# Kernel tuning notes

Hardware: AMD Instinct MI355X
Metric: run time of the kernel (lower is better)

The kernel has to match this reference:

```python
import jax, jax.numpy as jnp
import numpy as np

B, T, D, HD = 8, 2048, 1024, 64

def setup_inputs() -> dict:
    key = jax.random.key(0)
    k1, k2, k3, k4 = jax.random.split(key, 4)
    x = jax.random.normal(k1, (B, T, D), dtype=jnp.float32)
    Wq = jax.random.normal(k2, (D, HD), dtype=jnp.float32) * (D ** -0.5)
    Wk = jax.random.normal(k3, (D, HD), dtype=jnp.float32) * (D ** -0.5)
    Wv = jax.random.normal(k4, (D, HD), dtype=jnp.float32) * (D ** -0.5)
    return {"x": x, "Wq": Wq, "Wk": Wk, "Wv": Wv}

def reference(x, Wq, Wk, Wv):
    # x: [B,T,D]; projections: [D,HD]
    q = jnp.einsum('btd,dh->bth', x, Wq)
    k = jnp.einsum('btd,dh->bth', x, Wk)
    v = jnp.einsum('btd,dh->bth', x, Wv)
    hd = q.shape[-1]
    scores = jnp.einsum('bth,bsh->bts', q, k) * (hd ** -0.5)  # [B,T,T]
    t = scores.shape[-1]
    causal = jnp.tril(jnp.ones((t, t), dtype=bool))
    scores = jnp.where(causal, scores, -jnp.inf)
    w = jax.nn.softmax(scores, axis=-1)
    # dropout p=0.0 (eval) -> identity
    return jnp.einsum('bts,bsh->bth', w, v)
```

## Files before the change

### kernel.cpp

```cpp
#include <hip/hip_runtime.h>
#include <hip/hip_bf16.h>
#include <stdint.h>

#define NB 8
#define TT 2048
#define DD 1024
#define HDIM 64

typedef __bf16 bf16x8 __attribute__((ext_vector_type(8)));
typedef float f32x4 __attribute__((ext_vector_type(4)));

static_assert(sizeof(bf16x8) == 16, "bf16x8 must be 16 bytes");

__device__ inline ushort f2bf_bits(float f) {
    __hip_bfloat16 h = __float2bfloat16(f);
    return *reinterpret_cast<ushort*>(&h);
}
__device__ inline float bfbits2f(ushort u) {
    unsigned v = ((unsigned)u) << 16;
    return __builtin_bit_cast(float, v);
}
__device__ inline bf16x8 ldb8(const ushort* p) {
    return *reinterpret_cast<const bf16x8*>(p);
}

typedef __attribute__((address_space(3))) uint32_t lds_u32;
typedef const __attribute__((address_space(1))) uint32_t glb_u32;
__device__ inline void gl_lds16(const void* g, void* l) {
    __builtin_amdgcn_global_load_lds((glb_u32*)g, (lds_u32*)l, 16, 0, 0);
}

#define WCNT_VM2   0xF72
#define WCNT_VM3   0xF73
#define WCNT_VM4   0xF74
#define WCNT_LGKM0 0xC07F

__device__ inline int probe_f32(const ushort* x) {
    int lane = threadIdx.x & 63;
    int wild = 0;
    #pragma unroll
    for (int j = 0; j < 4; ++j) {
        ushort u = x[(lane * 4 + j) * 32];
        int e = (u >> 7) & 0xFF;
        wild += (e >= 0xC0);
    }
    unsigned long long m = __ballot(wild > 0);
    return __popcll(m) > 8;
}

__global__ __launch_bounds__(256) void k_wt(const ushort* __restrict__ x,
                                            const void* __restrict__ Wq,
                                            const void* __restrict__ Wk,
                                            const void* __restrict__ Wv,
                                            ushort* __restrict__ Wt) {
    int f32m = probe_f32(x);
    int idx = blockIdx.x * 256 + threadIdx.x;
    int mat = idx >> 16;
    int rem = idx & 65535;
    int d = rem >> 6;
    int h = rem & 63;
    const void* W = (mat == 0) ? Wq : (mat == 1) ? Wk : Wv;
    float v;
    if (f32m) v = ((const float*)W)[rem];
    else      v = bfbits2f(((const ushort*)W)[rem]);
    if (mat == 0) v *= 0.18033688011112042f;
    Wt[(size_t)mat * 65536 + (size_t)h * DD + d] = f2bf_bits(v);
}

template <int F32M>
__device__ inline void proj_body(const void* __restrict__ xv,
                                 const ushort* __restrict__ Wt,
                                 ushort* __restrict__ Qw,
                                 ushort* __restrict__ Kw,
                                 ushort* __restrict__ Vtw,
                                 ushort* Bf, float* Af) {
    int tid  = threadIdx.x;
    int w    = tid >> 6;
    int lane = tid & 63;
    int quad = lane >> 4;
    int col  = lane & 15;
    int mt   = w >> 2;
    int nh   = w & 3;
    int m0   = blockIdx.x * 32;

    ushort* Afb = (ushort*)Af;

    auto stage = [&](int buf, int kkk) {
        #pragma unroll
        for (int j = 0; j < 3; ++j) {
            int f  = w * 3 + j;
            int nt = f >> 1, ks = f & 1;
            gl_lds16(Wt + (size_t)(nt * 16 + col) * DD + kkk + ks * 32 + quad * 8,
                     Bf + ((size_t)buf * 24 + f) * 512);
        }
        if (F32M) {
            int amt = w >> 2, ks = (w >> 1) & 1, hf = w & 1;
            gl_lds16((const float*)xv + (size_t)(m0 + amt * 16 + col) * DD
                         + kkk + ks * 32 + hf * 4 + quad * 8,
                     Af + ((((buf * 2 + amt) * 2 + ks) * 2) + hf) * 256);
        } else if (w < 4) {
            int amt = w >> 1, ks = w & 1;
            gl_lds16((const ushort*)xv + (size_t)(m0 + amt * 16 + col) * DD
                         + kkk + ks * 32 + quad * 8,
                     Afb + (((buf * 2 + amt) * 2) + ks) * 512);
        }
    };

    f32x4 acc[3];
    #pragma unroll
    for (int i = 0; i < 3; ++i) acc[i] = (f32x4){0.f,0.f,0.f,0.f};

    stage(0, 0);
    for (int kk = 0; kk < DD; kk += 64) {
        int p  = (kk >> 6) & 1;
        int kn = (kk + 64 < DD) ? kk + 64 : kk;
        stage(p ^ 1, kn);
        if (F32M) {
            __builtin_amdgcn_s_waitcnt(WCNT_VM4);
        } else {
            if (w < 4) __builtin_amdgcn_s_waitcnt(WCNT_VM4);
            else       __builtin_amdgcn_s_waitcnt(WCNT_VM3);
        }
        __builtin_amdgcn_s_barrier();

        #pragma unroll
        for (int ks = 0; ks < 2; ++ks) {
            bf16x8 a;
            if (F32M) {
                f32x4 alo = *reinterpret_cast<const f32x4*>(Af + ((((p * 2 + mt) * 2 + ks) * 2) + 0) * 256 + lane * 4);
                f32x4 ahi = *reinterpret_cast<const f32x4*>(Af + ((((p * 2 + mt) * 2 + ks) * 2) + 1) * 256 + lane * 4);
                #pragma unroll
                for (int j = 0; j < 4; ++j) { a[j] = (__bf16)alo[j]; a[4+j] = (__bf16)ahi[j]; }
            } else {
                a = ldb8(Afb + (((p * 2 + mt) * 2) + ks) * 512 + lane * 8);
            }
            #pragma unroll
            for (int j = 0; j < 3; ++j) {
                int nt = nh * 3 + j;
                bf16x8 b = ldb8(Bf + ((size_t)p * 24 + nt * 2 + ks) * 512 + lane * 8);
                acc[j] = __builtin_amdgcn_mfma_f32_16x16x32_bf16(a, b, acc[j], 0, 0, 0);
            }
        }
        __builtin_amdgcn_s_waitcnt(WCNT_LGKM0);
        __builtin_amdgcn_s_barrier();
    }

    #pragma unroll
    for (int j = 0; j < 3; ++j) {
        int nt  = nh * 3 + j;
        int mat = nt >> 2;
        int h   = (nt & 3) * 16 + col;
        if (mat == 2) {
            #pragma unroll
            for (int r = 0; r < 4; ++r) {
                int row = m0 + mt * 16 + quad * 4 + r;
                int bb = row >> 11;
                int t  = row & (TT - 1);
                Vtw[(size_t)bb * HDIM * TT + (size_t)h * TT + t] = f2bf_bits(acc[j][r]);
            }
        } else {
            ushort* outp = (mat == 0) ? Qw : Kw;
            #pragma unroll
            for (int r = 0; r < 4; ++r) {
                int row = m0 + mt * 16 + quad * 4 + r;
                outp[(size_t)row * HDIM + h] = f2bf_bits(acc[j][r]);
            }
        }
    }
}

__global__ __launch_bounds__(512) void k_proj(const void* __restrict__ xv,
                                              const ushort* __restrict__ Wt,
                                              ushort* __restrict__ Qw,
                                              ushort* __restrict__ Kw,
                                              ushort* __restrict__ Vtw) {
    __shared__ ushort Bf[2 * 24 * 512];
    __shared__ float  Af[2 * 2 * 2 * 2 * 256];
    if (probe_f32((const ushort*)xv)) proj_body<1>(xv, Wt, Qw, Kw, Vtw, Bf, Af);
    else                              proj_body<0>(xv, Wt, Qw, Kw, Vtw, Bf, Af);
}

__global__ __launch_bounds__(256) void k_attn(const ushort* __restrict__ Qw,
                                              const ushort* __restrict__ Kw,
                                              const ushort* __restrict__ Vtw,
                                              ushort* __restrict__ Po,
                                              float* __restrict__ Pl) {
    int w    = threadIdx.x >> 6;
    int lane = threadIdx.x & 63;
    int quad = lane >> 4;
    int col  = lane & 15;
    int bid  = blockIdx.x;
    int b    = bid & 7;
    int idx  = 79 - (bid >> 3);
    int c, g;
    if (idx < 32)      { c = 0; g = idx; }
    else if (idx < 56) { c = 1; g = idx - 24; }
    else if (idx < 72) { c = 2; g = idx - 40; }
    else               { c = 3; g = idx - 48; }
    int qb = 4 * g + w;
    int m0 = qb * 16;
    int Bq = (qb < 32) ? qb : (qb < 64) ? 2*qb - 32 : (qb < 96) ? 3*qb - 96 : 4*qb - 192;
    int pid = b * 320 + Bq + c;

    const ushort* Qb = Qw + (size_t)b * TT * HDIM;
    const ushort* Kb = Kw + (size_t)b * TT * HDIM;
    const ushort* Vb = Vtw + (size_t)b * HDIM * TT;

    __shared__ ushort KVb[2][8][512];
    __shared__ __hip_bfloat16 Pls[4][16][40];

    auto stageKV = [&](int buf, int s) {
        #pragma unroll
        for (int j = 0; j < 2; ++j) {
            int f = w * 2 + j;
            const ushort* gp;
            if (f < 4) {
                int half = f & 1;
                int ro   = (f >> 1) * 16;
                gp = Kb + (size_t)(s + ro + col) * HDIM + half * 32 + quad * 8;
            } else {
                int vg = f - 4;
                gp = Vb + (size_t)(vg * 16 + col) * TT + s + quad * 8;
            }
            gl_lds16(gp, &KVb[buf][f][0]);
        }
    };

    bf16x8 qf0 = ldb8(Qb + (size_t)(m0 + col) * HDIM + quad * 8);
    bf16x8 qf1 = ldb8(Qb + (size_t)(m0 + col) * HDIM + 32 + quad * 8);

    f32x4 o0 = {0.f,0.f,0.f,0.f};
    f32x4 o1 = {0.f,0.f,0.f,0.f};
    f32x4 o2 = {0.f,0.f,0.f,0.f};
    f32x4 o3 = {0.f,0.f,0.f,0.f};
    float rsum[4] = {0.f, 0.f, 0.f, 0.f};

    const int start = c * 512;
    const int end   = min(start + 512, 64 * g + 64);

    stageKV(0, start);
    for (int s0 = start; s0 < end; s0 += 32) {
        int p  = ((s0 - start) >> 5) & 1;
        int sn = (s0 + 32 < end) ? s0 + 32 : s0;
        stageKV(p ^ 1, sn);
        __builtin_amdgcn_s_waitcnt(WCNT_VM2);
        __builtin_amdgcn_s_barrier();

        if (s0 < m0 + 16) {
            bf16x8 ck0l = ldb8(&KVb[p][0][lane * 8]);
            bf16x8 ck0h = ldb8(&KVb[p][1][lane * 8]);
            bf16x8 ck1l = ldb8(&KVb[p][2][lane * 8]);
            bf16x8 ck1h = ldb8(&KVb[p][3][lane * 8]);

            f32x4 S0 = {0.f,0.f,0.f,0.f};
            f32x4 S1 = {0.f,0.f,0.f,0.f};
            S0 = __builtin_amdgcn_mfma_f32_16x16x32_bf16(qf0, ck0l, S0, 0, 0, 0);
            S0 = __builtin_amdgcn_mfma_f32_16x16x32_bf16(qf1, ck0h, S0, 0, 0, 0);
            S1 = __builtin_amdgcn_mfma_f32_16x16x32_bf16(qf0, ck1l, S1, 0, 0, 0);
            S1 = __builtin_amdgcn_mfma_f32_16x16x32_bf16(qf1, ck1h, S1, 0, 0, 0);

            #pragma unroll
            for (int r = 0; r < 4; ++r) {
                int trow = m0 + quad * 4 + r;
                float aa = (s0 + col      > trow) ? -1e30f : S0[r];
                float dd = (s0 + 16 + col > trow) ? -1e30f : S1[r];
                float p0 = exp2f(aa);
                float p1 = exp2f(dd);
                rsum[r] += p0 + p1;
                Pls[w][quad * 4 + r][col]      = __float2bfloat16(p0);
                Pls[w][quad * 4 + r][16 + col] = __float2bfloat16(p1);
            }
            bf16x8 pf = *reinterpret_cast<const bf16x8*>(&Pls[w][col][quad * 8]);

            bf16x8 cv0 = ldb8(&KVb[p][4][lane * 8]);
            bf16x8 cv1 = ldb8(&KVb[p][5][lane * 8]);
            bf16x8 cv2 = ldb8(&KVb[p][6][lane * 8]);
            bf16x8 cv3 = ldb8(&KVb[p][7][lane * 8]);
            o0 = __builtin_amdgcn_mfma_f32_16x16x32_bf16(pf, cv0, o0, 0, 0, 0);
            o1 = __builtin_amdgcn_mfma_f32_16x16x32_bf16(pf, cv1, o1, 0, 0, 0);
            o2 = __builtin_amdgcn_mfma_f32_16x16x32_bf16(pf, cv2, o2, 0, 0, 0);
            o3 = __builtin_amdgcn_mfma_f32_16x16x32_bf16(pf, cv3, o3, 0, 0, 0);
        }
        __builtin_amdgcn_s_waitcnt(WCNT_LGKM0);
        __builtin_amdgcn_s_barrier();
    }

    #pragma unroll
    for (int off = 1; off < 16; off <<= 1) {
        #pragma unroll
        for (int r = 0; r < 4; ++r)
            rsum[r] += __shfl_xor(rsum[r], off, 64);
    }

    ushort* pb = Po + (size_t)pid * 1024;
    #pragma unroll
    for (int r = 0; r < 4; ++r) {
        int row = quad * 4 + r;
        pb[row * 64 + 0*16 + col] = f2bf_bits(o0[r]);
        pb[row * 64 + 1*16 + col] = f2bf_bits(o1[r]);
        pb[row * 64 + 2*16 + col] = f2bf_bits(o2[r]);
        pb[row * 64 + 3*16 + col] = f2bf_bits(o3[r]);
        if (col == 0) Pl[pid * 16 + row] = rsum[r];
    }
}

__global__ __launch_bounds__(256) void k_merge(const ushort* __restrict__ x,
                                               const ushort* __restrict__ Po,
                                               const float* __restrict__ Pl,
                                               void* __restrict__ outv) {
    int f32m = probe_f32(x);
    int wid  = blockIdx.x * 4 + (threadIdx.x >> 6);
    int lane = threadIdx.x & 63;
    int row  = lane >> 2;
    int g    = lane & 3;
    int b    = wid >> 7;
    int qb   = wid & 127;
    int nch  = (qb >> 5) + 1;
    int Bq   = (qb < 32) ? qb : (qb < 64) ? 2*qb - 32 : (qb < 96) ? 3*qb - 96 : 4*qb - 192;
    int pid0 = b * 320 + Bq;

    float L = 0.f;
    #pragma unroll
    for (int c = 0; c < 4; ++c)
        if (c < nch) L += Pl[(pid0 + c) * 16 + row];
    float inv = 1.0f / L;

    float o[16];
    #pragma unroll
    for (int j = 0; j < 16; ++j) o[j] = 0.f;
    #pragma unroll
    for (int c = 0; c < 4; ++c) {
        if (c < nch) {
            const ushort* p = Po + (size_t)(pid0 + c) * 1024 + row * 64 + g * 16;
            bf16x8 v0 = ldb8(p);
            bf16x8 v1 = ldb8(p + 8);
            #pragma unroll
            for (int j = 0; j < 8; ++j) {
                o[j]     += (float)v0[j];
                o[8 + j] += (float)v1[j];
            }
        }
    }

    size_t obase = ((size_t)b * TT + qb * 16 + row) * HDIM + g * 16;
    if (f32m) {
        float* ob = (float*)outv + obase;
        #pragma unroll
        for (int j = 0; j < 16; ++j) ob[j] = o[j] * inv;
    } else {
        ushort* ob = (ushort*)outv + obase;
        #pragma unroll
        for (int j = 0; j < 16; ++j) ob[j] = f2bf_bits(o[j] * inv);
    }
}

extern "C" void kernel_launch(void* const* d_in, const int* in_sizes, int n_in,
                              void* d_out, int out_size, void* d_ws, size_t ws_size,
                              hipStream_t stream) {
    const ushort* x = (const ushort*)d_in[0];
    ushort* Wt  = (ushort*)d_ws;
    ushort* Qw  = Wt + 3 * HDIM * DD;
    ushort* Kw  = Qw + (size_t)NB * TT * HDIM;
    ushort* Vtw = Kw + (size_t)NB * TT * HDIM;
    ushort* Po  = Vtw + (size_t)NB * TT * HDIM;
    float*  Pl  = (float*)(Po + (size_t)2560 * 1024);

    k_wt   <<<768, 256, 0, stream>>>(x, d_in[1], d_in[2], d_in[3], Wt);
    k_proj <<<512, 512, 0, stream>>>(d_in[0], Wt, Qw, Kw, Vtw);
    k_attn <<<640, 256, 0, stream>>>(Qw, Kw, Vtw, Po, Pl);
    k_merge<<<256, 256, 0, stream>>>(x, Po, Pl, d_out);
}
```

Before: 155.1 us.

## Load projection A-operand directly into registers and double rows per block

The QKV projection kernel stops staging x through LDS. Each wave now loads its A fragments straight from global memory into registers, prefetching the next k-step, while only the weight tiles stay in LDS. Each block covers 64 rows instead of 32, with every wave computing two 16-row tiles, so each weight tile read from LDS feeds twice as many MFMAs and the grid is halved. This cuts LDS traffic and reuses B better, at the cost of more registers, uncoalesced 16-byte global loads per lane, and fewer blocks to fill the GPU.

```diff
diff --git a/kernel.cpp b/kernel.cpp
--- a/kernel.cpp
+++ b/kernel.cpp
@@ -32,7 +32,6 @@
 
 #define WCNT_VM2   0xF72
 #define WCNT_VM3   0xF73
-#define WCNT_VM4   0xF74
 #define WCNT_LGKM0 0xC07F
 
 __device__ inline int probe_f32(const ushort* x) {
@@ -73,111 +72,134 @@
                                  ushort* __restrict__ Qw,
                                  ushort* __restrict__ Kw,
                                  ushort* __restrict__ Vtw,
-                                 ushort* Bf, float* Af) {
+                                 ushort* Bl) {
     int tid  = threadIdx.x;
     int w    = tid >> 6;
     int lane = tid & 63;
     int quad = lane >> 4;
     int col  = lane & 15;
-    int mt   = w >> 2;
+    int mt2  = w >> 2;
     int nh   = w & 3;
-    int m0   = blockIdx.x * 32;
-
-    ushort* Afb = (ushort*)Af;
-
-    auto stage = [&](int buf, int kkk) {
+    int m0   = blockIdx.x * 64;
+    int rbase = m0 + mt2 * 32;
+
+    const float*  xf = (const float*)xv;
+    const ushort* xb = (const ushort*)xv;
+
+    auto stageB = [&](int buf, int kkk) {
         #pragma unroll
         for (int j = 0; j < 3; ++j) {
             int f  = w * 3 + j;
             int nt = f >> 1, ks = f & 1;
             gl_lds16(Wt + (size_t)(nt * 16 + col) * DD + kkk + ks * 32 + quad * 8,
-                     Bf + ((size_t)buf * 24 + f) * 512);
-        }
-        if (F32M) {
-            int amt = w >> 2, ks = (w >> 1) & 1, hf = w & 1;
-            gl_lds16((const float*)xv + (size_t)(m0 + amt * 16 + col) * DD
-                         + kkk + ks * 32 + hf * 4 + quad * 8,
-                     Af + ((((buf * 2 + amt) * 2 + ks) * 2) + hf) * 256);
-        } else if (w < 4) {
-            int amt = w >> 1, ks = w & 1;
-            gl_lds16((const ushort*)xv + (size_t)(m0 + amt * 16 + col) * DD
-                         + kkk + ks * 32 + quad * 8,
-                     Afb + (((buf * 2 + amt) * 2) + ks) * 512);
+                     Bl + ((size_t)buf * 24 + f) * 512);
         }
     };
 
-    f32x4 acc[3];
-    #pragma unroll
-    for (int i = 0; i < 3; ++i) acc[i] = (f32x4){0.f,0.f,0.f,0.f};
-
-    stage(0, 0);
+    f32x4  aC[8];
+    bf16x8 aCb[4];
+
+    auto loadA = [&](int kkk) {
+        #pragma unroll
+        for (int mloc = 0; mloc < 2; ++mloc) {
+            #pragma unroll
+            for (int ks = 0; ks < 2; ++ks) {
+                size_t ro = (size_t)(rbase + mloc * 16 + col) * DD
+                          + kkk + ks * 32 + quad * 8;
+                if (F32M) {
+                    aC[(mloc * 2 + ks) * 2 + 0] = *reinterpret_cast<const f32x4*>(xf + ro);
+                    aC[(mloc * 2 + ks) * 2 + 1] = *reinterpret_cast<const f32x4*>(xf + ro + 4);
+                } else {
+                    aCb[mloc * 2 + ks] = ldb8(xb + ro);
+                }
+            }
+        }
+    };
+
+    f32x4 acc[2][3];
+    #pragma unroll
+    for (int i = 0; i < 2; ++i)
+        #pragma unroll
+        for (int j = 0; j < 3; ++j) acc[i][j] = (f32x4){0.f, 0.f, 0.f, 0.f};
+
+    stageB(0, 0);
+    loadA(0);
     for (int kk = 0; kk < DD; kk += 64) {
         int p  = (kk >> 6) & 1;
         int kn = (kk + 64 < DD) ? kk + 64 : kk;
-        stage(p ^ 1, kn);
+        stageB(p ^ 1, kn);
+        __builtin_amdgcn_s_waitcnt(WCNT_VM3);
+        __builtin_amdgcn_s_barrier();
+
+        bf16x8 af[4];
         if (F32M) {
-            __builtin_amdgcn_s_waitcnt(WCNT_VM4);
+            #pragma unroll
+            for (int i = 0; i < 4; ++i) {
+                f32x4 lo = aC[2 * i], hi = aC[2 * i + 1];
+                bf16x8 t;
+                #pragma unroll
+                for (int jj = 0; jj < 4; ++jj) {
+                    t[jj]     = (__bf16)lo[jj];
+                    t[4 + jj] = (__bf16)hi[jj];
+                }
+                af[i] = t;
+            }
         } else {
-            if (w < 4) __builtin_amdgcn_s_waitcnt(WCNT_VM4);
-            else       __builtin_amdgcn_s_waitcnt(WCNT_VM3);
-        }
-        __builtin_amdgcn_s_barrier();
+            #pragma unroll
+            for (int i = 0; i < 4; ++i) af[i] = aCb[i];
+        }
+        loadA(kn);
 
         #pragma unroll
         for (int ks = 0; ks < 2; ++ks) {
-            bf16x8 a;
-            if (F32M) {
-                f32x4 alo = *reinterpret_cast<const f32x4*>(Af + ((((p * 2 + mt) * 2 + ks) * 2) + 0) * 256 + lane * 4);
-                f32x4 ahi = *reinterpret_cast<const f32x4*>(Af + ((((p * 2 + mt) * 2 + ks) * 2) + 1) * 256 + lane * 4);
-                #pragma unroll
-                for (int j = 0; j < 4; ++j) { a[j] = (__bf16)alo[j]; a[4+j] = (__bf16)ahi[j]; }
-            } else {
-                a = ldb8(Afb + (((p * 2 + mt) * 2) + ks) * 512 + lane * 8);
-            }
             #pragma unroll
             for (int j = 0; j < 3; ++j) {
                 int nt = nh * 3 + j;
-                bf16x8 b = ldb8(Bf + ((size_t)p * 24 + nt * 2 + ks) * 512 + lane * 8);
-                acc[j] = __builtin_amdgcn_mfma_f32_16x16x32_bf16(a, b, acc[j], 0, 0, 0);
-            }
-        }
+                bf16x8 b = ldb8(Bl + ((size_t)p * 24 + nt * 2 + ks) * 512 + lane * 8);
+                acc[0][j] = __builtin_amdgcn_mfma_f32_16x16x32_bf16(af[0 * 2 + ks], b, acc[0][j], 0, 0, 0);
+                acc[1][j] = __builtin_amdgcn_mfma_f32_16x16x32_bf16(af[1 * 2 + ks], b, acc[1][j], 0, 0, 0);
+            }
+        }
+
         __builtin_amdgcn_s_waitcnt(WCNT_LGKM0);
         __builtin_amdgcn_s_barrier();
     }
 
     #pragma unroll
-    for (int j = 0; j < 3; ++j) {
-        int nt  = nh * 3 + j;
-        int mat = nt >> 2;
-        int h   = (nt & 3) * 16 + col;
-        if (mat == 2) {
-            #pragma unroll
-            for (int r = 0; r < 4; ++r) {
-                int row = m0 + mt * 16 + quad * 4 + r;
-                int bb = row >> 11;
-                int t  = row & (TT - 1);
-                Vtw[(size_t)bb * HDIM * TT + (size_t)h * TT + t] = f2bf_bits(acc[j][r]);
-            }
-        } else {
-            ushort* outp = (mat == 0) ? Qw : Kw;
-            #pragma unroll
-            for (int r = 0; r < 4; ++r) {
-                int row = m0 + mt * 16 + quad * 4 + r;
-                outp[(size_t)row * HDIM + h] = f2bf_bits(acc[j][r]);
-            }
-        }
-    }
-}
-
-__global__ __launch_bounds__(512) void k_proj(const void* __restrict__ xv,
-                                              const ushort* __restrict__ Wt,
-                                              ushort* __restrict__ Qw,
-                                              ushort* __restrict__ Kw,
-                                              ushort* __restrict__ Vtw) {
-    __shared__ ushort Bf[2 * 24 * 512];
-    __shared__ float  Af[2 * 2 * 2 * 2 * 256];
-    if (probe_f32((const ushort*)xv)) proj_body<1>(xv, Wt, Qw, Kw, Vtw, Bf, Af);
-    else                              proj_body<0>(xv, Wt, Qw, Kw, Vtw, Bf, Af);
+    for (int mloc = 0; mloc < 2; ++mloc) {
+        #pragma unroll
+        for (int j = 0; j < 3; ++j) {
+            int nt  = nh * 3 + j;
+            int mat = nt >> 2;
+            int h   = (nt & 3) * 16 + col;
+            if (mat == 2) {
+                #pragma unroll
+                for (int r = 0; r < 4; ++r) {
+                    int row = rbase + mloc * 16 + quad * 4 + r;
+                    int bb = row >> 11;
+                    int t  = row & (TT - 1);
+                    Vtw[(size_t)bb * HDIM * TT + (size_t)h * TT + t] = f2bf_bits(acc[mloc][j][r]);
+                }
+            } else {
+                ushort* outp = (mat == 0) ? Qw : Kw;
+                #pragma unroll
+                for (int r = 0; r < 4; ++r) {
+                    int row = rbase + mloc * 16 + quad * 4 + r;
+                    outp[(size_t)row * HDIM + h] = f2bf_bits(acc[mloc][j][r]);
+                }
+            }
+        }
+    }
+}
+
+__global__ __launch_bounds__(512, 4) void k_proj(const void* __restrict__ xv,
+                                                 const ushort* __restrict__ Wt,
+                                                 ushort* __restrict__ Qw,
+                                                 ushort* __restrict__ Kw,
+                                                 ushort* __restrict__ Vtw) {
+    __shared__ ushort Bl[2 * 24 * 512];
+    if (probe_f32((const ushort*)xv)) proj_body<1>(xv, Wt, Qw, Kw, Vtw, Bl);
+    else                              proj_body<0>(xv, Wt, Qw, Kw, Vtw, Bl);
 }
 
 __global__ __launch_bounds__(256) void k_attn(const ushort* __restrict__ Qw,
@@ -366,7 +388,7 @@
     float*  Pl  = (float*)(Po + (size_t)2560 * 1024);
 
     k_wt   <<<768, 256, 0, stream>>>(x, d_in[1], d_in[2], d_in[3], Wt);
-    k_proj <<<512, 512, 0, stream>>>(d_in[0], Wt, Qw, Kw, Vtw);
+    k_proj <<<256, 512, 0, stream>>>(d_in[0], Wt, Qw, Kw, Vtw);
     k_attn <<<640, 256, 0, stream>>>(Qw, Kw, Vtw, Po, Pl);
     k_merge<<<256, 256, 0, stream>>>(x, Po, Pl, d_out);
 }
```

Result: slower. 172.7 us (+11.4%).

## Widen attention KV tile to 64 keys with triple-buffered LDS staging

Applied to the files above, without the earlier changes.

The attention kernel now processes 64 keys per loop step instead of 32, and stages K/V tiles three buffers deep with a prefetch distance of two. The wait count is raised to match the extra loads in flight, and the launch bounds ask for two blocks per CU. The aim is to halve the barrier and synchronisation count per key and hide more global-load latency behind the MFMA work. In exchange, LDS use grows to roughly 57 KB per block, which may limit occupancy. Causal-diagonal tiles also waste more masked work at the coarser granularity.

```diff
diff --git a/kernel.cpp b/kernel.cpp
--- a/kernel.cpp
+++ b/kernel.cpp
@@ -30,9 +30,9 @@
     __builtin_amdgcn_global_load_lds((glb_u32*)g, (lds_u32*)l, 16, 0, 0);
 }
 
-#define WCNT_VM2   0xF72
 #define WCNT_VM3   0xF73
 #define WCNT_VM4   0xF74
+#define WCNT_VM8   0xF78
 #define WCNT_LGKM0 0xC07F
 
 __device__ inline int probe_f32(const ushort* x) {
@@ -180,11 +180,11 @@
     else                              proj_body<0>(xv, Wt, Qw, Kw, Vtw, Bf, Af);
 }
 
-__global__ __launch_bounds__(256) void k_attn(const ushort* __restrict__ Qw,
-                                              const ushort* __restrict__ Kw,
-                                              const ushort* __restrict__ Vtw,
-                                              ushort* __restrict__ Po,
-                                              float* __restrict__ Pl) {
+__global__ __launch_bounds__(256, 2) void k_attn(const ushort* __restrict__ Qw,
+                                                 const ushort* __restrict__ Kw,
+                                                 const ushort* __restrict__ Vtw,
+                                                 ushort* __restrict__ Po,
+                                                 float* __restrict__ Pl) {
     int w    = threadIdx.x >> 6;
     int lane = threadIdx.x & 63;
     int quad = lane >> 4;
@@ -206,21 +206,23 @@
     const ushort* Kb = Kw + (size_t)b * TT * HDIM;
     const ushort* Vb = Vtw + (size_t)b * HDIM * TT;
 
-    __shared__ ushort KVb[2][8][512];
-    __shared__ __hip_bfloat16 Pls[4][16][40];
+    __shared__ ushort KVb[3][16][512];
+    __shared__ ushort Pls[4][16][72];
 
     auto stageKV = [&](int buf, int s) {
         #pragma unroll
-        for (int j = 0; j < 2; ++j) {
-            int f = w * 2 + j;
+        for (int j = 0; j < 4; ++j) {
+            int f = w * 4 + j;
             const ushort* gp;
-            if (f < 4) {
+            if (f < 8) {
+                int ksub = f >> 1;
                 int half = f & 1;
-                int ro   = (f >> 1) * 16;
-                gp = Kb + (size_t)(s + ro + col) * HDIM + half * 32 + quad * 8;
+                gp = Kb + (size_t)(s + ksub * 16 + col) * HDIM + half * 32 + quad * 8;
             } else {
-                int vg = f - 4;
-                gp = Vb + (size_t)(vg * 16 + col) * TT + s + quad * 8;
+                int vf   = f - 8;
+                int hsub = vf >> 1;
+                int kh   = vf & 1;
+                gp = Vb + (size_t)(hsub * 16 + col) * TT + s + kh * 32 + quad * 8;
             }
             gl_lds16(gp, &KVb[buf][f][0]);
         }
@@ -229,57 +231,58 @@
     bf16x8 qf0 = ldb8(Qb + (size_t)(m0 + col) * HDIM + quad * 8);
     bf16x8 qf1 = ldb8(Qb + (size_t)(m0 + col) * HDIM + 32 + quad * 8);
 
-    f32x4 o0 = {0.f,0.f,0.f,0.f};
-    f32x4 o1 = {0.f,0.f,0.f,0.f};
-    f32x4 o2 = {0.f,0.f,0.f,0.f};
-    f32x4 o3 = {0.f,0.f,0.f,0.f};
+    f32x4 o[4];
+    #pragma unroll
+    for (int i = 0; i < 4; ++i) o[i] = (f32x4){0.f,0.f,0.f,0.f};
     float rsum[4] = {0.f, 0.f, 0.f, 0.f};
 
-    const int start = c * 512;
-    const int end   = min(start + 512, 64 * g + 64);
+    const int start  = c * 512;
+    const int end    = min(start + 512, 64 * g + 64);
+    const int nsteps = (end - start) >> 6;
 
     stageKV(0, start);
-    for (int s0 = start; s0 < end; s0 += 32) {
-        int p  = ((s0 - start) >> 5) & 1;
-        int sn = (s0 + 32 < end) ? s0 + 32 : s0;
-        stageKV(p ^ 1, sn);
-        __builtin_amdgcn_s_waitcnt(WCNT_VM2);
+    stageKV(1, (nsteps > 1) ? start + 64 : start);
+    for (int t = 0; t < nsteps; ++t) {
+        int s0 = start + t * 64;
+        int p  = t % 3;
+        int s2 = (t + 2 < nsteps) ? s0 + 128 : s0;
+        stageKV((p + 2) % 3, s2);
+        __builtin_amdgcn_s_waitcnt(WCNT_VM8);
         __builtin_amdgcn_s_barrier();
 
         if (s0 < m0 + 16) {
-            bf16x8 ck0l = ldb8(&KVb[p][0][lane * 8]);
-            bf16x8 ck0h = ldb8(&KVb[p][1][lane * 8]);
-            bf16x8 ck1l = ldb8(&KVb[p][2][lane * 8]);
-            bf16x8 ck1h = ldb8(&KVb[p][3][lane * 8]);
-
-            f32x4 S0 = {0.f,0.f,0.f,0.f};
-            f32x4 S1 = {0.f,0.f,0.f,0.f};
-            S0 = __builtin_amdgcn_mfma_f32_16x16x32_bf16(qf0, ck0l, S0, 0, 0, 0);
-            S0 = __builtin_amdgcn_mfma_f32_16x16x32_bf16(qf1, ck0h, S0, 0, 0, 0);
-            S1 = __builtin_amdgcn_mfma_f32_16x16x32_bf16(qf0, ck1l, S1, 0, 0, 0);
-            S1 = __builtin_amdgcn_mfma_f32_16x16x32_bf16(qf1, ck1h, S1, 0, 0, 0);
+            f32x4 S[4];
+            #pragma unroll
+            for (int sub = 0; sub < 4; ++sub) {
+                bf16x8 kl = ldb8(&KVb[p][sub * 2 + 0][lane * 8]);
+                bf16x8 kh = ldb8(&KVb[p][sub * 2 + 1][lane * 8]);
+                f32x4 s = {0.f,0.f,0.f,0.f};
+                s = __builtin_amdgcn_mfma_f32_16x16x32_bf16(qf0, kl, s, 0, 0, 0);
+                s = __builtin_amdgcn_mfma_f32_16x16x32_bf16(qf1, kh, s, 0, 0, 0);
+                S[sub] = s;
+            }
 
             #pragma unroll
             for (int r = 0; r < 4; ++r) {
                 int trow = m0 + quad * 4 + r;
-                float aa = (s0 + col      > trow) ? -1e30f : S0[r];
-                float dd = (s0 + 16 + col > trow) ? -1e30f : S1[r];
-                float p0 = exp2f(aa);
-                float p1 = exp2f(dd);
-                rsum[r] += p0 + p1;
-                Pls[w][quad * 4 + r][col]      = __float2bfloat16(p0);
-                Pls[w][quad * 4 + r][16 + col] = __float2bfloat16(p1);
-            }
-            bf16x8 pf = *reinterpret_cast<const bf16x8*>(&Pls[w][col][quad * 8]);
-
-            bf16x8 cv0 = ldb8(&KVb[p][4][lane * 8]);
-            bf16x8 cv1 = ldb8(&KVb[p][5][lane * 8]);
-            bf16x8 cv2 = ldb8(&KVb[p][6][lane * 8]);
-            bf16x8 cv3 = ldb8(&KVb[p][7][lane * 8]);
-            o0 = __builtin_amdgcn_mfma_f32_16x16x32_bf16(pf, cv0, o0, 0, 0, 0);
-            o1 = __builtin_amdgcn_mfma_f32_16x16x32_bf16(pf, cv1, o1, 0, 0, 0);
-            o2 = __builtin_amdgcn_mfma_f32_16x16x32_bf16(pf, cv2, o2, 0, 0, 0);
-            o3 = __builtin_amdgcn_mfma_f32_16x16x32_bf16(pf, cv3, o3, 0, 0, 0);
+                #pragma unroll
+                for (int sub = 0; sub < 4; ++sub) {
+                    float vv = (s0 + sub * 16 + col > trow) ? -1e30f : S[sub][r];
+                    float pp = exp2f(vv);
+                    rsum[r] += pp;
+                    Pls[w][quad * 4 + r][sub * 16 + col] = f2bf_bits(pp);
+                }
+            }
+            bf16x8 pf0 = ldb8(&Pls[w][col][quad * 8]);
+            bf16x8 pf1 = ldb8(&Pls[w][col][32 + quad * 8]);
+
+            #pragma unroll
+            for (int hsub = 0; hsub < 4; ++hsub) {
+                bf16x8 v0 = ldb8(&KVb[p][8 + hsub * 2 + 0][lane * 8]);
+                bf16x8 v1 = ldb8(&KVb[p][8 + hsub * 2 + 1][lane * 8]);
+                o[hsub] = __builtin_amdgcn_mfma_f32_16x16x32_bf16(pf0, v0, o[hsub], 0, 0, 0);
+                o[hsub] = __builtin_amdgcn_mfma_f32_16x16x32_bf16(pf1, v1, o[hsub], 0, 0, 0);
+            }
         }
         __builtin_amdgcn_s_waitcnt(WCNT_LGKM0);
         __builtin_amdgcn_s_barrier();
@@ -296,10 +299,10 @@
     #pragma unroll
     for (int r = 0; r < 4; ++r) {
         int row = quad * 4 + r;
-        pb[row * 64 + 0*16 + col] = f2bf_bits(o0[r]);
-        pb[row * 64 + 1*16 + col] = f2bf_bits(o1[r]);
-        pb[row * 64 + 2*16 + col] = f2bf_bits(o2[r]);
-        pb[row * 64 + 3*16 + col] = f2bf_bits(o3[r]);
+        pb[row * 64 + 0*16 + col] = f2bf_bits(o[0][r]);
+        pb[row * 64 + 1*16 + col] = f2bf_bits(o[1][r]);
+        pb[row * 64 + 2*16 + col] = f2bf_bits(o[2][r]);
+        pb[row * 64 + 3*16 + col] = f2bf_bits(o[3][r]);
         if (col == 0) Pl[pid * 16 + row] = rsum[r];
     }
 }
```

Result: slower. 159.4 us (+2.8%).

## Load K/V fragments directly from global memory, dropping shared-memory staging and barriers

Applied to the files above, without the earlier changes.

The attention kernel no longer stages K and V tiles cooperatively into double-buffered shared memory with barriers. Each wave now loads its own K and V MFMA fragments straight from global memory and runs only the tiles it needs under the causal bound, so waves no longer synchronize with each other. This removes block-wide barriers and idle waves past their causal limit. In exchange each wave re-reads K/V that the block's four waves used to share, raising global and L2 traffic, and there is no explicit prefetch to hide load latency.

```diff
diff --git a/kernel.cpp b/kernel.cpp
--- a/kernel.cpp
+++ b/kernel.cpp
@@ -30,7 +30,6 @@
     __builtin_amdgcn_global_load_lds((glb_u32*)g, (lds_u32*)l, 16, 0, 0);
 }
 
-#define WCNT_VM2   0xF72
 #define WCNT_VM3   0xF73
 #define WCNT_VM4   0xF74
 #define WCNT_LGKM0 0xC07F
@@ -206,25 +205,7 @@
     const ushort* Kb = Kw + (size_t)b * TT * HDIM;
     const ushort* Vb = Vtw + (size_t)b * HDIM * TT;
 
-    __shared__ ushort KVb[2][8][512];
-    __shared__ __hip_bfloat16 Pls[4][16][40];
-
-    auto stageKV = [&](int buf, int s) {
-        #pragma unroll
-        for (int j = 0; j < 2; ++j) {
-            int f = w * 2 + j;
-            const ushort* gp;
-            if (f < 4) {
-                int half = f & 1;
-                int ro   = (f >> 1) * 16;
-                gp = Kb + (size_t)(s + ro + col) * HDIM + half * 32 + quad * 8;
-            } else {
-                int vg = f - 4;
-                gp = Vb + (size_t)(vg * 16 + col) * TT + s + quad * 8;
-            }
-            gl_lds16(gp, &KVb[buf][f][0]);
-        }
-    };
+    __shared__ ushort Pls[4][16][40];
 
     bf16x8 qf0 = ldb8(Qb + (size_t)(m0 + col) * HDIM + quad * 8);
     bf16x8 qf1 = ldb8(Qb + (size_t)(m0 + col) * HDIM + 32 + quad * 8);
@@ -236,53 +217,47 @@
     float rsum[4] = {0.f, 0.f, 0.f, 0.f};
 
     const int start = c * 512;
-    const int end   = min(start + 512, 64 * g + 64);
-
-    stageKV(0, start);
-    for (int s0 = start; s0 < end; s0 += 32) {
-        int p  = ((s0 - start) >> 5) & 1;
-        int sn = (s0 + 32 < end) ? s0 + 32 : s0;
-        stageKV(p ^ 1, sn);
-        __builtin_amdgcn_s_waitcnt(WCNT_VM2);
-        __builtin_amdgcn_s_barrier();
-
-        if (s0 < m0 + 16) {
-            bf16x8 ck0l = ldb8(&KVb[p][0][lane * 8]);
-            bf16x8 ck0h = ldb8(&KVb[p][1][lane * 8]);
-            bf16x8 ck1l = ldb8(&KVb[p][2][lane * 8]);
-            bf16x8 ck1h = ldb8(&KVb[p][3][lane * 8]);
-
-            f32x4 S0 = {0.f,0.f,0.f,0.f};
-            f32x4 S1 = {0.f,0.f,0.f,0.f};
-            S0 = __builtin_amdgcn_mfma_f32_16x16x32_bf16(qf0, ck0l, S0, 0, 0, 0);
-            S0 = __builtin_amdgcn_mfma_f32_16x16x32_bf16(qf1, ck0h, S0, 0, 0, 0);
-            S1 = __builtin_amdgcn_mfma_f32_16x16x32_bf16(qf0, ck1l, S1, 0, 0, 0);
-            S1 = __builtin_amdgcn_mfma_f32_16x16x32_bf16(qf1, ck1h, S1, 0, 0, 0);
-
-            #pragma unroll
-            for (int r = 0; r < 4; ++r) {
-                int trow = m0 + quad * 4 + r;
-                float aa = (s0 + col      > trow) ? -1e30f : S0[r];
-                float dd = (s0 + 16 + col > trow) ? -1e30f : S1[r];
-                float p0 = exp2f(aa);
-                float p1 = exp2f(dd);
-                rsum[r] += p0 + p1;
-                Pls[w][quad * 4 + r][col]      = __float2bfloat16(p0);
-                Pls[w][quad * 4 + r][16 + col] = __float2bfloat16(p1);
-            }
-            bf16x8 pf = *reinterpret_cast<const bf16x8*>(&Pls[w][col][quad * 8]);
-
-            bf16x8 cv0 = ldb8(&KVb[p][4][lane * 8]);
-            bf16x8 cv1 = ldb8(&KVb[p][5][lane * 8]);
-            bf16x8 cv2 = ldb8(&KVb[p][6][lane * 8]);
-            bf16x8 cv3 = ldb8(&KVb[p][7][lane * 8]);
-            o0 = __builtin_amdgcn_mfma_f32_16x16x32_bf16(pf, cv0, o0, 0, 0, 0);
-            o1 = __builtin_amdgcn_mfma_f32_16x16x32_bf16(pf, cv1, o1, 0, 0, 0);
-            o2 = __builtin_amdgcn_mfma_f32_16x16x32_bf16(pf, cv2, o2, 0, 0, 0);
-            o3 = __builtin_amdgcn_mfma_f32_16x16x32_bf16(pf, cv3, o3, 0, 0, 0);
-        }
-        __builtin_amdgcn_s_waitcnt(WCNT_LGKM0);
-        __builtin_amdgcn_s_barrier();
+    const int nst   = (min(start + 512, m0 + 16) - start + 31) >> 5;
+
+    for (int t = 0; t < nst; ++t) {
+        int s0 = start + t * 32;
+
+        const ushort* kp = Kb + (size_t)(s0 + col) * HDIM + quad * 8;
+        bf16x8 ck0l = ldb8(kp);
+        bf16x8 ck0h = ldb8(kp + 32);
+        bf16x8 ck1l = ldb8(kp + (size_t)16 * HDIM);
+        bf16x8 ck1h = ldb8(kp + (size_t)16 * HDIM + 32);
+
+        const ushort* vp = Vb + (size_t)col * TT + s0 + quad * 8;
+        bf16x8 cv0 = ldb8(vp);
+        bf16x8 cv1 = ldb8(vp + (size_t)16 * TT);
+        bf16x8 cv2 = ldb8(vp + (size_t)32 * TT);
+        bf16x8 cv3 = ldb8(vp + (size_t)48 * TT);
+
+        f32x4 S0 = {0.f,0.f,0.f,0.f};
+        f32x4 S1 = {0.f,0.f,0.f,0.f};
+        S0 = __builtin_amdgcn_mfma_f32_16x16x32_bf16(qf0, ck0l, S0, 0, 0, 0);
+        S0 = __builtin_amdgcn_mfma_f32_16x16x32_bf16(qf1, ck0h, S0, 0, 0, 0);
+        S1 = __builtin_amdgcn_mfma_f32_16x16x32_bf16(qf0, ck1l, S1, 0, 0, 0);
+        S1 = __builtin_amdgcn_mfma_f32_16x16x32_bf16(qf1, ck1h, S1, 0, 0, 0);
+
+        #pragma unroll
+        for (int r = 0; r < 4; ++r) {
+            int trow = m0 + quad * 4 + r;
+            float aa = (s0 + col      > trow) ? -1e30f : S0[r];
+            float dd = (s0 + 16 + col > trow) ? -1e30f : S1[r];
+            float p0 = exp2f(aa);
+            float p1 = exp2f(dd);
+            rsum[r] += p0 + p1;
+            Pls[w][quad * 4 + r][col]      = f2bf_bits(p0);
+            Pls[w][quad * 4 + r][16 + col] = f2bf_bits(p1);
+        }
+        bf16x8 pf = ldb8(&Pls[w][col][quad * 8]);
+
+        o0 = __builtin_amdgcn_mfma_f32_16x16x32_bf16(pf, cv0, o0, 0, 0, 0);
+        o1 = __builtin_amdgcn_mfma_f32_16x16x32_bf16(pf, cv1, o1, 0, 0, 0);
+        o2 = __builtin_amdgcn_mfma_f32_16x16x32_bf16(pf, cv2, o2, 0, 0, 0);
+        o3 = __builtin_amdgcn_mfma_f32_16x16x32_bf16(pf, cv3, o3, 0, 0, 0);
     }
 
     #pragma unroll
```

Result: slower. 179.9 us (+16.0%).
